# Kernel optimization log

Measured on AMD Instinct MI355X. Metric: run time of the kernel, lower is better.

Reference implementation:

```python
import jax, jax.numpy as jnp
import numpy as np

ALPHA = 0.2        # LeakyReLU negative slope (config['alpha'])
NEG_INF = -9e15    # mask value from the original code


def setup_inputs() -> dict:
    key = jax.random.key(0)
    k1, k2, k3, k4 = jax.random.split(key, 4)
    N, Fin, Fout = 8192, 512, 256
    inp = jax.random.normal(k1, (N, Fin), dtype=jnp.float32)
    adj = jax.random.randint(k2, (N, N), 0, 2, dtype=jnp.int32)
    # xavier_uniform with gain=1.414
    limW = 1.414 * np.sqrt(6.0 / (Fin + Fout))
    W = jax.random.uniform(k3, (Fin, Fout), dtype=jnp.float32, minval=-limW, maxval=limW)
    lima = 1.414 * np.sqrt(6.0 / (2 * Fout + 1))
    a = jax.random.uniform(k4, (2 * Fout, 1), dtype=jnp.float32, minval=-lima, maxval=lima)
    return {"input": inp, "adj": adj, "W": W, "a": a}


def reference(input, adj, W, a):
    # h: [N, F]
    h = input @ W
    Fout = W.shape[1]
    # The original builds a_input[i, j] = concat(h_i, h_j) and dots with a.
    # Equivalently: e_ij = leakyrelu(h_i . a[:F] + h_j . a[F:]), computed
    # without the O(N^2 * 2F) intermediate.
    s1 = h @ a[:Fout, 0]   # [N] contribution from node i
    s2 = h @ a[Fout:, 0]   # [N] contribution from node j
    e = s1[:, None] + s2[None, :]                     # [N, N]
    e = jnp.where(e > 0, e, ALPHA * e)                # LeakyReLU
    scores = jnp.where(adj > 0, e, NEG_INF)
    attention = jax.nn.softmax(scores, axis=1)        # row-wise softmax
    # dropout is identity in inference mode (training=False)
    h_prime = attention @ h                           # [N, F]
    return jax.nn.elu(h_prime)                        # concat=True path
```

## Files before the change

kernel.cpp:

```cpp
#include <hip/hip_runtime.h>
#include <stdint.h>
#include <stddef.h>


#define N_NODES 8192
#define FIN     512
#define FOUT    256
#define LRALPHA 0.2f
#define MI_SHIFT 16.0f

typedef float f32x4 __attribute__((ext_vector_type(4)));
typedef short s16x8 __attribute__((ext_vector_type(8)));
typedef unsigned short u16x4 __attribute__((ext_vector_type(4)));
typedef int   i32x4 __attribute__((ext_vector_type(4)));
typedef unsigned long long u64;

typedef const uint32_t __attribute__((address_space(1)))* gas1_u32;
typedef uint32_t __attribute__((address_space(3)))* las3_u32;

__device__ __forceinline__ short f2bf_rne(float f) {
  uint32_t u = __builtin_bit_cast(uint32_t, f);
  u += 0x7fffu + ((u >> 16) & 1u);
  return (short)(u >> 16);
}
__device__ __forceinline__ short f2bf_fast(float f) {
  uint32_t u = __builtin_bit_cast(uint32_t, f);
  return (short)((u + 0x8000u) >> 16);
}
__device__ __forceinline__ float bf2f(short s) {
  uint32_t u = ((uint32_t)(uint16_t)s) << 16;
  return __builtin_bit_cast(float, u);
}

__global__ __launch_bounds__(256) void k_prep(const float* __restrict__ W,
                                              uint16_t* __restrict__ WThi,
                                              uint16_t* __restrict__ WTlo) {
  const int idx = blockIdx.x * 256 + threadIdx.x;
  const int n = idx >> 9;
  const int k = idx & 511;
  float v = W[k * FOUT + n];
  short h = f2bf_rne(v);
  WThi[idx] = (uint16_t)h;
  WTlo[idx] = (uint16_t)f2bf_rne(v - bf2f(h));
}

__global__ __launch_bounds__(256, 4) void k_pre(const float* __restrict__ X,
                                                const uint16_t* __restrict__ WThi,
                                                const uint16_t* __restrict__ WTlo,
                                                const float* __restrict__ a,
                                                uint16_t* __restrict__ HTf,
                                                float* __restrict__ s1g,
                                                float* __restrict__ s2g) {
  __shared__ float ls1[16], ls2[16];
  __shared__ uint16_t tile[FOUT * 16];
  const int lane = threadIdx.x & 63;
  const int w    = threadIdx.x >> 6;

  const int m    = lane & 15;
  const int quad = lane >> 4;
  const int i0   = blockIdx.x * 16;
  const int colg = w * 64;

  f32x4 acc[4];
#pragma unroll
  for (int cb = 0; cb < 4; ++cb) { f32x4 z = {0.f,0.f,0.f,0.f}; acc[cb] = z; }

  for (int kt = 0; kt < FIN / 32; ++kt) {
    const int k0 = kt * 32 + quad * 8;
    const float* ap = X + (size_t)(i0 + m) * FIN + k0;
    f32x4 a0 = *(const f32x4*)ap;
    f32x4 a1 = *(const f32x4*)(ap + 4);
    s16x8 ahi, alo;
#pragma unroll
    for (int e = 0; e < 4; ++e) {
      short h0 = f2bf_rne(a0[e]); ahi[e] = h0; alo[e] = f2bf_rne(a0[e] - bf2f(h0));
      short h1 = f2bf_rne(a1[e]); ahi[4+e] = h1; alo[4+e] = f2bf_rne(a1[e] - bf2f(h1));
    }
#pragma unroll
    for (int cb = 0; cb < 4; ++cb) {
      const int n = colg + cb * 16 + m;
      s16x8 bhi = *(const s16x8*)(WThi + (size_t)n * FIN + k0);
      s16x8 blo = *(const s16x8*)(WTlo + (size_t)n * FIN + k0);
      acc[cb] = __builtin_amdgcn_mfma_f32_16x16x32_bf16(ahi, bhi, acc[cb], 0, 0, 0);
      acc[cb] = __builtin_amdgcn_mfma_f32_16x16x32_bf16(ahi, blo, acc[cb], 0, 0, 0);
      acc[cb] = __builtin_amdgcn_mfma_f32_16x16x32_bf16(alo, bhi, acc[cb], 0, 0, 0);
    }
  }

  float p1[4] = {0.f,0.f,0.f,0.f}, p2[4] = {0.f,0.f,0.f,0.f};
#pragma unroll
  for (int cb = 0; cb < 4; ++cb) {
    const int n = colg + cb * 16 + m;
    const float a1c = a[n];
    const float a2c = a[FOUT + n];
#pragma unroll
    for (int reg = 0; reg < 4; ++reg) {
      p1[reg] += acc[cb][reg] * a1c;
      p2[reg] += acc[cb][reg] * a2c;
    }
  }
#pragma unroll
  for (int off = 1; off <= 8; off <<= 1)
#pragma unroll
    for (int reg = 0; reg < 4; ++reg) {
      p1[reg] += __shfl_xor(p1[reg], off);
      p2[reg] += __shfl_xor(p2[reg], off);
    }
  if (threadIdx.x < 16) { ls1[threadIdx.x] = 0.f; ls2[threadIdx.x] = 0.f; }
  __syncthreads();
  if (m == 0) {
#pragma unroll
    for (int reg = 0; reg < 4; ++reg) {
      atomicAdd(&ls1[quad * 4 + reg], p1[reg]);
      atomicAdd(&ls2[quad * 4 + reg], p2[reg]);
    }
  }
#pragma unroll
  for (int cb = 0; cb < 4; ++cb) {
    const int col = colg + cb * 16 + m;
    u16x4 pk;
#pragma unroll
    for (int reg = 0; reg < 4; ++reg) pk[reg] = (uint16_t)f2bf_rne(acc[cb][reg]);
    *(u16x4*)(tile + col * 16 + quad * 4) = pk;
  }
  __syncthreads();
  const int t = threadIdx.x;
  if (t < 16) { s1g[i0 + t] = ls1[t]; s2g[i0 + t] = ls2[t]; }
  const int jt = i0 >> 5;
  const int qh = (i0 >> 4) & 1;
  const int c  = t >> 4;
  const int mm = t & 15;
#pragma unroll
  for (int qq = 0; qq < 2; ++qq) {
    uint4 v = *(const uint4*)(tile + (c * 16 + mm) * 16 + qq * 8);
    *(uint4*)(HTf + ((((size_t)jt * 16 + c) * 64) + (qh * 2 + qq) * 16 + mm) * 8) = v;
  }
}

__global__ __launch_bounds__(512, 4) void k_attn(const uint16_t* __restrict__ HTf,
                                                 const float* __restrict__ s1,
                                                 const float* __restrict__ s2,
                                                 const int* __restrict__ adj,
                                                 float* __restrict__ pout,
                                                 float* __restrict__ pden,
                                                 int split) {
  __shared__ uint16_t PL[2][4096];
  __shared__ uint16_t BL[2][8192];
  __shared__ float lss2[1024];
  __shared__ float ldsden[512];

  const int tid  = threadIdx.x;
  const int lane = tid & 63;
  const int w    = tid >> 6;
  const int m    = lane & 15;
  const int q    = lane >> 4;
  const int rg   = w >> 2, cg = w & 3;
  const int rr   = tid >> 2;
  const int cw   = tid & 3;
  const int i0   = blockIdx.x * 128;
  const int sp   = blockIdx.y;
  const int jrange = N_NODES / split;
  const int jbeg   = sp * jrange;
  const int jblk   = jbeg >> 5;
  const int nphase = jrange / 32;

  const float s1r = s1[i0 + rr];
  float mi = fmaxf(s1r + MI_SHIFT, LRALPHA * (s1r + MI_SHIFT));

  f32x4 acc[4][4];
#pragma unroll
  for (int rt = 0; rt < 4; ++rt)
#pragma unroll
    for (int cb = 0; cb < 4; ++cb) { f32x4 z = {0.f,0.f,0.f,0.f}; acc[rt][cb] = z; }
  float den = 0.f;

  const int* adjp = adj + (size_t)(i0 + rr) * N_NODES + jbeg + cw * 8;
  i32x4 A0a = *(const i32x4*)adjp;
  i32x4 A0b = *(const i32x4*)(adjp + 4);
  i32x4 A1a = *(const i32x4*)(adjp + 32);
  i32x4 A1b = *(const i32x4*)(adjp + 36);

#define STAGE_B(pp, buf) do {                                                  \
    const uint16_t* s_ = HTf + (((size_t)(jblk + (pp))) << 13) + (w << 10) +   \
                         (lane << 3);                                          \
    __builtin_amdgcn_global_load_lds((gas1_u32)(const void*)s_,                \
        (las3_u32)(void*)(&BL[buf][w << 10]), 16, 0, 0);                       \
    __builtin_amdgcn_global_load_lds((gas1_u32)(const void*)(s_ + 512),        \
        (las3_u32)(void*)(&BL[buf][(w << 10) + 512]), 16, 0, 0);               \
  } while (0)

  STAGE_B(0, 0);

#pragma unroll 1
  for (int p = 0; p < nphase; ++p) {
    if ((p & 31) == 0) {
      __syncthreads();
      if (tid < 256) *(f32x4*)(lss2 + tid * 4) =
        *(const f32x4*)(s2 + jbeg + (p >> 5) * 1024 + tid * 4);
      __syncthreads();
    }
    const int pl = p & 31;
    f32x4 sA = *(const f32x4*)(lss2 + pl * 32 + cw * 8);
    f32x4 sB = *(const f32x4*)(lss2 + pl * 32 + cw * 8 + 4);
    s16x8 P0;
#pragma unroll
    for (int e = 0; e < 4; ++e) {
      float x0 = s1r + sA[e];
      float pv0 = __expf(fmaxf(x0, LRALPHA * x0) - mi);
      pv0 = A0a[e] ? pv0 : 0.f;
      den += pv0; P0[e] = f2bf_fast(pv0);
      float x1 = s1r + sB[e];
      float pv1 = __expf(fmaxf(x1, LRALPHA * x1) - mi);
      pv1 = A0b[e] ? pv1 : 0.f;
      den += pv1; P0[4 + e] = f2bf_fast(pv1);
    }
    *(s16x8*)(PL[p & 1] + (cw * 128 + rr) * 8) = P0;
    __syncthreads();
    i32x4 A2a = {0,0,0,0}, A2b = {0,0,0,0};
    if (p + 2 < nphase) {
      const int* np = adjp + (size_t)(p + 2) * 32;
      A2a = *(const i32x4*)np;
      A2b = *(const i32x4*)(np + 4);
    }
    if (p + 1 < nphase) STAGE_B(p + 1, (p + 1) & 1);
    s16x8 F[4];
#pragma unroll
    for (int rt = 0; rt < 4; ++rt)
      F[rt] = *(const s16x8*)(PL[p & 1] + (q * 128 + rg * 64 + rt * 16 + m) * 8);
    __builtin_amdgcn_s_setprio(1);
#pragma unroll
    for (int cb = 0; cb < 4; ++cb) {
      s16x8 Bv = *(const s16x8*)(&BL[p & 1][((cg * 4 + cb) << 9) + (lane << 3)]);
#pragma unroll
      for (int rt = 0; rt < 4; ++rt)
        acc[rt][cb] = __builtin_amdgcn_mfma_f32_16x16x32_bf16(Bv, F[rt], acc[rt][cb], 0, 0, 0);
    }
    __builtin_amdgcn_s_setprio(0);
    A0a = A1a; A0b = A1b; A1a = A2a; A1b = A2b;
  }
#undef STAGE_B

  ldsden[cw * 128 + rr] = den;
  __syncthreads();
  if (tid < 128) {
    float d = ldsden[tid] + ldsden[128 + tid] + ldsden[256 + tid] + ldsden[384 + tid];
    pden[(size_t)sp * N_NODES + i0 + tid] = d;
  }
#pragma unroll
  for (int rt = 0; rt < 4; ++rt)
#pragma unroll
    for (int cb = 0; cb < 4; ++cb) {
      const int row = i0 + rg * 64 + rt * 16 + m;
      const int col = cg * 64 + cb * 16 + q * 4;
      *(f32x4*)(pout + ((size_t)sp * N_NODES + row) * FOUT + col) = acc[rt][cb];
    }
}

__global__ __launch_bounds__(256) void k_reduce(const float* __restrict__ pout,
                                                const float* __restrict__ pden,
                                                float* __restrict__ out,
                                                int split) {
  const int gid = blockIdx.x * 256 + threadIdx.x;
  const int i = gid >> 6;
  const int c = (gid & 63) << 2;
  f32x4 sum = {0.f,0.f,0.f,0.f};
  float den = 0.f;
  for (int s = 0; s < split; ++s) {
    sum += *(const f32x4*)(pout + ((size_t)s * N_NODES + i) * FOUT + c);
    den += pden[(size_t)s * N_NODES + i];
  }
  const float inv = 1.0f / den;
  f32x4 r;
#pragma unroll
  for (int e = 0; e < 4; ++e) {
    float v = sum[e] * inv;
    r[e] = v > 0.f ? v : (__expf(v) - 1.0f);
  }
  *(f32x4*)(out + (size_t)i * FOUT + c) = r;
}

extern "C" void kernel_launch(void* const* d_in, const int* in_sizes, int n_in,
                              void* d_out, int out_size, void* d_ws, size_t ws_size,
                              hipStream_t stream) {
  const float* X   = (const float*)d_in[0];
  const int*   adj = (const int*)d_in[1];
  const float* W   = (const float*)d_in[2];
  const float* a   = (const float*)d_in[3];
  float* out = (float*)d_out;

  char* ws = (char*)d_ws;
  uint16_t* HTf  = (uint16_t*)ws;
  uint16_t* WThi = (uint16_t*)(ws + (4u << 20));
  uint16_t* WTlo = (uint16_t*)(ws + (4u << 20) + 262144);
  float*    s1   = (float*)(ws + (4u << 20) + 524288);
  float*    s2   = s1 + N_NODES;
  float*    pden = s2 + N_NODES;
  const size_t pout_off = (size_t)16u << 20;
  const size_t slab = (size_t)N_NODES * FOUT * sizeof(float);

  int split;
  if      (ws_size >= pout_off + 8 * slab) split = 8;
  else if (ws_size >= pout_off + 4 * slab) split = 4;
  else if (ws_size >= pout_off + 2 * slab) split = 2;
  else                                     split = 1;
  float* pout = (split == 1) ? out : (float*)(ws + pout_off);

  k_prep<<<dim3(512), dim3(256), 0, stream>>>(W, WThi, WTlo);
  k_pre<<<dim3(512), dim3(256), 0, stream>>>(X, WThi, WTlo, a, HTf, s1, s2);
  k_attn<<<dim3(N_NODES / 128, split), dim3(512), 0, stream>>>(HTf, s1, s2, adj, pout, pden, split);
  k_reduce<<<dim3(N_NODES * FOUT / 4 / 256), dim3(256), 0, stream>>>(pout, pden, out, split);
}
```

Before: 465.0 us.

## Halve attention row tile to 64 rows and reduce split-K to 4

Each attention block now covers 64 rows instead of 128, with 8 threads per row each computing 4 probabilities. The denominator reduction moves from shared memory to warp shuffles. The maximum j-split drops from 8 to 4, so the reduce kernel combines fewer partial slabs. The smaller tile doubles the number of row blocks and lowers register and LDS pressure, but each block reuses the staged HT tile across half as many rows, which doubles total HT traffic.

```diff
diff --git a/kernel.cpp b/kernel.cpp
--- a/kernel.cpp
+++ b/kernel.cpp
@@ -144,10 +144,9 @@
                                                  float* __restrict__ pout,
                                                  float* __restrict__ pden,
                                                  int split) {
-  __shared__ uint16_t PL[2][4096];
+  __shared__ uint16_t PL[2][2048];
   __shared__ uint16_t BL[2][8192];
   __shared__ float lss2[1024];
-  __shared__ float ldsden[512];
 
   const int tid  = threadIdx.x;
   const int lane = tid & 63;
@@ -155,9 +154,9 @@
   const int m    = lane & 15;
   const int q    = lane >> 4;
   const int rg   = w >> 2, cg = w & 3;
-  const int rr   = tid >> 2;
-  const int cw   = tid & 3;
-  const int i0   = blockIdx.x * 128;
+  const int rr   = tid >> 3;
+  const int cw   = tid & 7;
+  const int i0   = blockIdx.x * 64;
   const int sp   = blockIdx.y;
   const int jrange = N_NODES / split;
   const int jbeg   = sp * jrange;
@@ -167,18 +166,16 @@
   const float s1r = s1[i0 + rr];
   float mi = fmaxf(s1r + MI_SHIFT, LRALPHA * (s1r + MI_SHIFT));
 
-  f32x4 acc[4][4];
-#pragma unroll
-  for (int rt = 0; rt < 4; ++rt)
+  f32x4 acc[2][4];
+#pragma unroll
+  for (int rt = 0; rt < 2; ++rt)
 #pragma unroll
     for (int cb = 0; cb < 4; ++cb) { f32x4 z = {0.f,0.f,0.f,0.f}; acc[rt][cb] = z; }
   float den = 0.f;
 
-  const int* adjp = adj + (size_t)(i0 + rr) * N_NODES + jbeg + cw * 8;
-  i32x4 A0a = *(const i32x4*)adjp;
-  i32x4 A0b = *(const i32x4*)(adjp + 4);
-  i32x4 A1a = *(const i32x4*)(adjp + 32);
-  i32x4 A1b = *(const i32x4*)(adjp + 36);
+  const int* adjp = adj + (size_t)(i0 + rr) * N_NODES + jbeg + cw * 4;
+  i32x4 A0 = *(const i32x4*)adjp;
+  i32x4 A1 = *(const i32x4*)(adjp + 32);
 
 #define STAGE_B(pp, buf) do {                                                  \
     const uint16_t* s_ = HTf + (((size_t)(jblk + (pp))) << 13) + (w << 10) +   \
@@ -200,57 +197,47 @@
       __syncthreads();
     }
     const int pl = p & 31;
-    f32x4 sA = *(const f32x4*)(lss2 + pl * 32 + cw * 8);
-    f32x4 sB = *(const f32x4*)(lss2 + pl * 32 + cw * 8 + 4);
-    s16x8 P0;
+    f32x4 sA = *(const f32x4*)(lss2 + pl * 32 + cw * 4);
+    u16x4 P0;
 #pragma unroll
     for (int e = 0; e < 4; ++e) {
       float x0 = s1r + sA[e];
       float pv0 = __expf(fmaxf(x0, LRALPHA * x0) - mi);
-      pv0 = A0a[e] ? pv0 : 0.f;
-      den += pv0; P0[e] = f2bf_fast(pv0);
-      float x1 = s1r + sB[e];
-      float pv1 = __expf(fmaxf(x1, LRALPHA * x1) - mi);
-      pv1 = A0b[e] ? pv1 : 0.f;
-      den += pv1; P0[4 + e] = f2bf_fast(pv1);
-    }
-    *(s16x8*)(PL[p & 1] + (cw * 128 + rr) * 8) = P0;
+      pv0 = A0[e] ? pv0 : 0.f;
+      den += pv0; P0[e] = (uint16_t)f2bf_fast(pv0);
+    }
+    *(u16x4*)(PL[p & 1] + (((cw >> 1) * 64 + rr) * 8) + (cw & 1) * 4) = P0;
     __syncthreads();
-    i32x4 A2a = {0,0,0,0}, A2b = {0,0,0,0};
-    if (p + 2 < nphase) {
-      const int* np = adjp + (size_t)(p + 2) * 32;
-      A2a = *(const i32x4*)np;
-      A2b = *(const i32x4*)(np + 4);
-    }
+    i32x4 A2 = {0,0,0,0};
+    if (p + 2 < nphase) A2 = *(const i32x4*)(adjp + (size_t)(p + 2) * 32);
     if (p + 1 < nphase) STAGE_B(p + 1, (p + 1) & 1);
-    s16x8 F[4];
-#pragma unroll
-    for (int rt = 0; rt < 4; ++rt)
-      F[rt] = *(const s16x8*)(PL[p & 1] + (q * 128 + rg * 64 + rt * 16 + m) * 8);
+    s16x8 F[2];
+#pragma unroll
+    for (int rt = 0; rt < 2; ++rt)
+      F[rt] = *(const s16x8*)(PL[p & 1] + (q * 64 + rg * 32 + rt * 16 + m) * 8);
     __builtin_amdgcn_s_setprio(1);
 #pragma unroll
     for (int cb = 0; cb < 4; ++cb) {
       s16x8 Bv = *(const s16x8*)(&BL[p & 1][((cg * 4 + cb) << 9) + (lane << 3)]);
 #pragma unroll
-      for (int rt = 0; rt < 4; ++rt)
+      for (int rt = 0; rt < 2; ++rt)
         acc[rt][cb] = __builtin_amdgcn_mfma_f32_16x16x32_bf16(Bv, F[rt], acc[rt][cb], 0, 0, 0);
     }
     __builtin_amdgcn_s_setprio(0);
-    A0a = A1a; A0b = A1b; A1a = A2a; A1b = A2b;
+    A0 = A1; A1 = A2;
   }
 #undef STAGE_B
 
-  ldsden[cw * 128 + rr] = den;
-  __syncthreads();
-  if (tid < 128) {
-    float d = ldsden[tid] + ldsden[128 + tid] + ldsden[256 + tid] + ldsden[384 + tid];
-    pden[(size_t)sp * N_NODES + i0 + tid] = d;
-  }
-#pragma unroll
-  for (int rt = 0; rt < 4; ++rt)
+  den += __shfl_xor(den, 1);
+  den += __shfl_xor(den, 2);
+  den += __shfl_xor(den, 4);
+  if (cw == 0) pden[(size_t)sp * N_NODES + i0 + rr] = den;
+
+#pragma unroll
+  for (int rt = 0; rt < 2; ++rt)
 #pragma unroll
     for (int cb = 0; cb < 4; ++cb) {
-      const int row = i0 + rg * 64 + rt * 16 + m;
+      const int row = i0 + rg * 32 + rt * 16 + m;
       const int col = cg * 64 + cb * 16 + q * 4;
       *(f32x4*)(pout + ((size_t)sp * N_NODES + row) * FOUT + col) = acc[rt][cb];
     }
@@ -299,14 +286,13 @@
   const size_t slab = (size_t)N_NODES * FOUT * sizeof(float);
 
   int split;
-  if      (ws_size >= pout_off + 8 * slab) split = 8;
-  else if (ws_size >= pout_off + 4 * slab) split = 4;
+  if      (ws_size >= pout_off + 4 * slab) split = 4;
   else if (ws_size >= pout_off + 2 * slab) split = 2;
   else                                     split = 1;
   float* pout = (split == 1) ? out : (float*)(ws + pout_off);
 
   k_prep<<<dim3(512), dim3(256), 0, stream>>>(W, WThi, WTlo);
   k_pre<<<dim3(512), dim3(256), 0, stream>>>(X, WThi, WTlo, a, HTf, s1, s2);
-  k_attn<<<dim3(N_NODES / 128, split), dim3(512), 0, stream>>>(HTf, s1, s2, adj, pout, pden, split);
+  k_attn<<<dim3(N_NODES / 64, split), dim3(512), 0, stream>>>(HTf, s1, s2, adj, pout, pden, split);
   k_reduce<<<dim3(N_NODES * FOUT / 4 / 256), dim3(256), 0, stream>>>(pout, pden, out, split);
 }
```

New measurement: 458.7 us. Within noise of the previous version (-1.4%).

## Drop LDS staging in attention kernel; each wave owns 16 rows, streams H from global

Applied to the files above, without the earlier changes.

Rewrites the attention kernel so each wave handles 16 rows across all 256 output columns. The wave computes its own probability fragment in registers and reads the H^T tile fragments directly from global memory, with no LDS and no block barriers. The goal is to remove the __syncthreads and LDS round-trips per phase. In exchange, every wave re-reads the full H tile from global/L2 (4x less reuse per block), the per-wave accumulator state grows to 16 tiles, and the launch shape changes to 256-thread blocks with a 1-D grid.

```diff
diff --git a/kernel.cpp b/kernel.cpp
--- a/kernel.cpp
+++ b/kernel.cpp
@@ -13,10 +13,6 @@
 typedef short s16x8 __attribute__((ext_vector_type(8)));
 typedef unsigned short u16x4 __attribute__((ext_vector_type(4)));
 typedef int   i32x4 __attribute__((ext_vector_type(4)));
-typedef unsigned long long u64;
-
-typedef const uint32_t __attribute__((address_space(1)))* gas1_u32;
-typedef uint32_t __attribute__((address_space(3)))* las3_u32;
 
 __device__ __forceinline__ short f2bf_rne(float f) {
   uint32_t u = __builtin_bit_cast(uint32_t, f);
@@ -137,123 +133,116 @@
   }
 }
 
-__global__ __launch_bounds__(512, 4) void k_attn(const uint16_t* __restrict__ HTf,
+__global__ __launch_bounds__(256, 3) void k_attn(const uint16_t* __restrict__ HTf,
                                                  const float* __restrict__ s1,
                                                  const float* __restrict__ s2,
                                                  const int* __restrict__ adj,
                                                  float* __restrict__ pout,
                                                  float* __restrict__ pden,
                                                  int split) {
-  __shared__ uint16_t PL[2][4096];
-  __shared__ uint16_t BL[2][8192];
-  __shared__ float lss2[1024];
-  __shared__ float ldsden[512];
-
   const int tid  = threadIdx.x;
   const int lane = tid & 63;
   const int w    = tid >> 6;
   const int m    = lane & 15;
   const int q    = lane >> 4;
-  const int rg   = w >> 2, cg = w & 3;
-  const int rr   = tid >> 2;
-  const int cw   = tid & 3;
-  const int i0   = blockIdx.x * 128;
-  const int sp   = blockIdx.y;
+  const int rowgrp = blockIdx.x & 127;
+  const int sp     = blockIdx.x >> 7;
+  const int i0   = rowgrp * 64 + w * 16;
   const int jrange = N_NODES / split;
   const int jbeg   = sp * jrange;
   const int jblk   = jbeg >> 5;
   const int nphase = jrange / 32;
 
-  const float s1r = s1[i0 + rr];
-  float mi = fmaxf(s1r + MI_SHIFT, LRALPHA * (s1r + MI_SHIFT));
-
-  f32x4 acc[4][4];
-#pragma unroll
-  for (int rt = 0; rt < 4; ++rt)
-#pragma unroll
-    for (int cb = 0; cb < 4; ++cb) { f32x4 z = {0.f,0.f,0.f,0.f}; acc[rt][cb] = z; }
+  const float s1r = s1[i0 + m];
+  const float mi = fmaxf(s1r + MI_SHIFT, LRALPHA * (s1r + MI_SHIFT));
+
+  f32x4 acc[16];
+#pragma unroll
+  for (int cb = 0; cb < 16; ++cb) { f32x4 z = {0.f,0.f,0.f,0.f}; acc[cb] = z; }
   float den = 0.f;
 
-  const int* adjp = adj + (size_t)(i0 + rr) * N_NODES + jbeg + cw * 8;
+  const int* adjp = adj + (size_t)(i0 + m) * N_NODES + jbeg + q * 8;
+  const float* s2p = s2 + jbeg + q * 8;
+  const uint16_t* HTb = HTf + ((size_t)jblk << 13) + lane * 8;
+
   i32x4 A0a = *(const i32x4*)adjp;
   i32x4 A0b = *(const i32x4*)(adjp + 4);
   i32x4 A1a = *(const i32x4*)(adjp + 32);
   i32x4 A1b = *(const i32x4*)(adjp + 36);
-
-#define STAGE_B(pp, buf) do {                                                  \
-    const uint16_t* s_ = HTf + (((size_t)(jblk + (pp))) << 13) + (w << 10) +   \
-                         (lane << 3);                                          \
-    __builtin_amdgcn_global_load_lds((gas1_u32)(const void*)s_,                \
-        (las3_u32)(void*)(&BL[buf][w << 10]), 16, 0, 0);                       \
-    __builtin_amdgcn_global_load_lds((gas1_u32)(const void*)(s_ + 512),        \
-        (las3_u32)(void*)(&BL[buf][(w << 10) + 512]), 16, 0, 0);               \
-  } while (0)
-
-  STAGE_B(0, 0);
+  f32x4 sc0 = *(const f32x4*)s2p;
+  f32x4 sc1 = *(const f32x4*)(s2p + 4);
 
 #pragma unroll 1
   for (int p = 0; p < nphase; ++p) {
-    if ((p & 31) == 0) {
-      __syncthreads();
-      if (tid < 256) *(f32x4*)(lss2 + tid * 4) =
-        *(const f32x4*)(s2 + jbeg + (p >> 5) * 1024 + tid * 4);
-      __syncthreads();
-    }
-    const int pl = p & 31;
-    f32x4 sA = *(const f32x4*)(lss2 + pl * 32 + cw * 8);
-    f32x4 sB = *(const f32x4*)(lss2 + pl * 32 + cw * 8 + 4);
-    s16x8 P0;
-#pragma unroll
-    for (int e = 0; e < 4; ++e) {
-      float x0 = s1r + sA[e];
-      float pv0 = __expf(fmaxf(x0, LRALPHA * x0) - mi);
-      pv0 = A0a[e] ? pv0 : 0.f;
-      den += pv0; P0[e] = f2bf_fast(pv0);
-      float x1 = s1r + sB[e];
-      float pv1 = __expf(fmaxf(x1, LRALPHA * x1) - mi);
-      pv1 = A0b[e] ? pv1 : 0.f;
-      den += pv1; P0[4 + e] = f2bf_fast(pv1);
-    }
-    *(s16x8*)(PL[p & 1] + (cw * 128 + rr) * 8) = P0;
-    __syncthreads();
+    const uint16_t* hb = HTb + ((size_t)p << 13);
+    s16x8 BvA0 = *(const s16x8*)(hb);
+    s16x8 BvA1 = *(const s16x8*)(hb + 512);
+    s16x8 BvA2 = *(const s16x8*)(hb + 1024);
+    s16x8 BvA3 = *(const s16x8*)(hb + 1536);
     i32x4 A2a = {0,0,0,0}, A2b = {0,0,0,0};
     if (p + 2 < nphase) {
       const int* np = adjp + (size_t)(p + 2) * 32;
       A2a = *(const i32x4*)np;
       A2b = *(const i32x4*)(np + 4);
     }
-    if (p + 1 < nphase) STAGE_B(p + 1, (p + 1) & 1);
-    s16x8 F[4];
-#pragma unroll
-    for (int rt = 0; rt < 4; ++rt)
-      F[rt] = *(const s16x8*)(PL[p & 1] + (q * 128 + rg * 64 + rt * 16 + m) * 8);
-    __builtin_amdgcn_s_setprio(1);
-#pragma unroll
-    for (int cb = 0; cb < 4; ++cb) {
-      s16x8 Bv = *(const s16x8*)(&BL[p & 1][((cg * 4 + cb) << 9) + (lane << 3)]);
-#pragma unroll
-      for (int rt = 0; rt < 4; ++rt)
-        acc[rt][cb] = __builtin_amdgcn_mfma_f32_16x16x32_bf16(Bv, F[rt], acc[rt][cb], 0, 0, 0);
-    }
-    __builtin_amdgcn_s_setprio(0);
+    f32x4 sn0 = {0.f,0.f,0.f,0.f}, sn1 = sn0;
+    if (p + 1 < nphase) {
+      const float* nsp = s2p + (size_t)(p + 1) * 32;
+      sn0 = *(const f32x4*)nsp;
+      sn1 = *(const f32x4*)(nsp + 4);
+    }
+    s16x8 F;
+#pragma unroll
+    for (int e = 0; e < 4; ++e) {
+      float x0 = s1r + sc0[e];
+      float pv0 = __expf(fmaxf(x0, LRALPHA * x0) - mi);
+      pv0 = A0a[e] ? pv0 : 0.f;
+      den += pv0; F[e] = f2bf_fast(pv0);
+      float x1 = s1r + sc1[e];
+      float pv1 = __expf(fmaxf(x1, LRALPHA * x1) - mi);
+      pv1 = A0b[e] ? pv1 : 0.f;
+      den += pv1; F[4 + e] = f2bf_fast(pv1);
+    }
+    s16x8 BvB0 = *(const s16x8*)(hb + 2048);
+    s16x8 BvB1 = *(const s16x8*)(hb + 2560);
+    s16x8 BvB2 = *(const s16x8*)(hb + 3072);
+    s16x8 BvB3 = *(const s16x8*)(hb + 3584);
+    acc[0] = __builtin_amdgcn_mfma_f32_16x16x32_bf16(BvA0, F, acc[0], 0, 0, 0);
+    acc[1] = __builtin_amdgcn_mfma_f32_16x16x32_bf16(BvA1, F, acc[1], 0, 0, 0);
+    acc[2] = __builtin_amdgcn_mfma_f32_16x16x32_bf16(BvA2, F, acc[2], 0, 0, 0);
+    acc[3] = __builtin_amdgcn_mfma_f32_16x16x32_bf16(BvA3, F, acc[3], 0, 0, 0);
+    BvA0 = *(const s16x8*)(hb + 4096);
+    BvA1 = *(const s16x8*)(hb + 4608);
+    BvA2 = *(const s16x8*)(hb + 5120);
+    BvA3 = *(const s16x8*)(hb + 5632);
+    acc[4] = __builtin_amdgcn_mfma_f32_16x16x32_bf16(BvB0, F, acc[4], 0, 0, 0);
+    acc[5] = __builtin_amdgcn_mfma_f32_16x16x32_bf16(BvB1, F, acc[5], 0, 0, 0);
+    acc[6] = __builtin_amdgcn_mfma_f32_16x16x32_bf16(BvB2, F, acc[6], 0, 0, 0);
+    acc[7] = __builtin_amdgcn_mfma_f32_16x16x32_bf16(BvB3, F, acc[7], 0, 0, 0);
+    BvB0 = *(const s16x8*)(hb + 6144);
+    BvB1 = *(const s16x8*)(hb + 6656);
+    BvB2 = *(const s16x8*)(hb + 7168);
+    BvB3 = *(const s16x8*)(hb + 7680);
+    acc[8]  = __builtin_amdgcn_mfma_f32_16x16x32_bf16(BvA0, F, acc[8],  0, 0, 0);
+    acc[9]  = __builtin_amdgcn_mfma_f32_16x16x32_bf16(BvA1, F, acc[9],  0, 0, 0);
+    acc[10] = __builtin_amdgcn_mfma_f32_16x16x32_bf16(BvA2, F, acc[10], 0, 0, 0);
+    acc[11] = __builtin_amdgcn_mfma_f32_16x16x32_bf16(BvA3, F, acc[11], 0, 0, 0);
+    acc[12] = __builtin_amdgcn_mfma_f32_16x16x32_bf16(BvB0, F, acc[12], 0, 0, 0);
+    acc[13] = __builtin_amdgcn_mfma_f32_16x16x32_bf16(BvB1, F, acc[13], 0, 0, 0);
+    acc[14] = __builtin_amdgcn_mfma_f32_16x16x32_bf16(BvB2, F, acc[14], 0, 0, 0);
+    acc[15] = __builtin_amdgcn_mfma_f32_16x16x32_bf16(BvB3, F, acc[15], 0, 0, 0);
     A0a = A1a; A0b = A1b; A1a = A2a; A1b = A2b;
-  }
-#undef STAGE_B
-
-  ldsden[cw * 128 + rr] = den;
-  __syncthreads();
-  if (tid < 128) {
-    float d = ldsden[tid] + ldsden[128 + tid] + ldsden[256 + tid] + ldsden[384 + tid];
-    pden[(size_t)sp * N_NODES + i0 + tid] = d;
-  }
-#pragma unroll
-  for (int rt = 0; rt < 4; ++rt)
-#pragma unroll
-    for (int cb = 0; cb < 4; ++cb) {
-      const int row = i0 + rg * 64 + rt * 16 + m;
-      const int col = cg * 64 + cb * 16 + q * 4;
-      *(f32x4*)(pout + ((size_t)sp * N_NODES + row) * FOUT + col) = acc[rt][cb];
-    }
+    sc0 = sn0; sc1 = sn1;
+  }
+
+  den += __shfl_xor(den, 16);
+  den += __shfl_xor(den, 32);
+  if (lane < 16) pden[(size_t)sp * N_NODES + i0 + m] = den;
+
+  float* po = pout + ((size_t)sp * N_NODES + i0 + m) * FOUT + q * 4;
+#pragma unroll
+  for (int cb = 0; cb < 16; ++cb)
+    *(f32x4*)(po + cb * 16) = acc[cb];
 }
 
 __global__ __launch_bounds__(256) void k_reduce(const float* __restrict__ pout,
@@ -307,6 +296,6 @@
 
   k_prep<<<dim3(512), dim3(256), 0, stream>>>(W, WThi, WTlo);
   k_pre<<<dim3(512), dim3(256), 0, stream>>>(X, WThi, WTlo, a, HTf, s1, s2);
-  k_attn<<<dim3(N_NODES / 128, split), dim3(512), 0, stream>>>(HTf, s1, s2, adj, pout, pden, split);
+  k_attn<<<dim3(128 * split), dim3(256), 0, stream>>>(HTf, s1, s2, adj, pout, pden, split);
   k_reduce<<<dim3(N_NODES * FOUT / 4 / 256), dim3(256), 0, stream>>>(pout, pden, out, split);
 }
```

New measurement: 572.4 us. 23.1% more time.
